# Optimization experiments

Measured on AMD Instinct MI355X. Metric: run time of the kernel, lower is better.

The kernel has to match this reference:

```python
import jax, jax.numpy as jnp
import numpy as np

B, A, N, G, F = 16, 256, 64, 64, 128  # batch, atoms, neighbors, gaussians, filters
CUTOFF = 5.0


def ssp(x):
    # shifted softplus: ln(0.5*e^x + 0.5)
    return jax.nn.softplus(x) - jnp.log(2.0).astype(x.dtype)


def setup_inputs() -> dict:
    key = jax.random.key(0)
    ks = jax.random.split(key, 10)
    x = jax.random.normal(ks[0], (B, A, F), jnp.float32)
    r_ij = jax.random.uniform(ks[1], (B, A, N), jnp.float32) * 6.0  # some beyond cutoff
    f_ij = jax.random.uniform(ks[2], (B, A, N, G), jnp.float32)  # gaussian-expanded dists
    neighbors = jax.random.randint(ks[3], (B, A, N), 0, A)
    pairwise_mask = (jax.random.uniform(ks[4], (B, A, N)) < 0.9).astype(jnp.float32)
    s = lambda fan: 1.0 / np.sqrt(fan)
    fw1 = jax.random.normal(ks[5], (G, F), jnp.float32) * s(G)
    fb1 = jnp.zeros((F,), jnp.float32)
    fw2 = jax.random.normal(ks[6], (F, F), jnp.float32) * s(F)
    fb2 = jnp.zeros((F,), jnp.float32)
    w_in2f = jax.random.normal(ks[7], (F, F), jnp.float32) * s(F)
    w_f2out = jax.random.normal(ks[8], (F, F), jnp.float32) * s(F)
    b_f2out = jnp.zeros((F,), jnp.float32)
    return {"x": x, "r_ij": r_ij, "f_ij": f_ij, "neighbors": neighbors,
            "pairwise_mask": pairwise_mask, "fw1": fw1, "fb1": fb1, "fw2": fw2,
            "fb2": fb2, "w_in2f": w_in2f, "w_f2out": w_f2out, "b_f2out": b_f2out}


def reference(x, r_ij, f_ij, neighbors, pairwise_mask,
              fw1, fb1, fw2, fb2, w_in2f, w_f2out, b_f2out):
    # filter network: Dense(G->F, ssp) -> Dense(F->F)
    W = ssp(jnp.einsum('bang,gf->banf', f_ij, fw1) + fb1)
    W = jnp.einsum('banf,fh->banh', W, fw2) + fb2  # [B,A,N,F]
    # cosine cutoff
    C = 0.5 * (jnp.cos(r_ij * (jnp.pi / CUTOFF)) + 1.0)
    C = C * (r_ij < CUTOFF).astype(r_ij.dtype)
    W = W * C[..., None]
    # in2f (no bias), then gather neighbor features along atom axis
    y = jnp.einsum('bad,df->baf', x, w_in2f)  # [B,A,F]
    bidx = jnp.arange(y.shape[0])[:, None, None]
    y_nbh = y[bidx, neighbors]  # [B,A,N,F]
    # filter-weight multiply + masked sum aggregate over neighbor axis
    y = jnp.sum(y_nbh * W * pairwise_mask[..., None], axis=2)  # [B,A,F]
    # f2out with shifted-softplus activation
    return ssp(jnp.einsum('baf,fo->bao', y, w_f2out) + b_f2out)
```

## Files before the change

kernel.cpp:

```cpp
#include <hip/hip_runtime.h>
#include <hip/hip_bf16.h>
#include <math.h>

#define B_ 16
#define A_ 256
#define N_ 64
#define G_ 64
#define F_ 128

typedef __attribute__((ext_vector_type(8))) short short8;
typedef __attribute__((ext_vector_type(4))) float floatx4;

__device__ __forceinline__ float ssp(float x) {
    const float t = __expf(-fabsf(x));
    return fmaxf(x, 0.0f) + __logf(1.0f + t) - 0.69314718055994531f;
}
__device__ __forceinline__ unsigned short f2bf(float f) {
    union { float f; unsigned u; } v; v.f = f;
    v.u += 0x7fffu + ((v.u >> 16) & 1u);
    return (unsigned short)(v.u >> 16);
}
__device__ __forceinline__ float bf2f(unsigned short u) {
    union { unsigned i; float f; } v;
    v.i = ((unsigned)u) << 16;
    return v.f;
}

__global__ __launch_bounds__(256) void k1_prep_in2f(
    const float* __restrict__ x,   const float* __restrict__ win,
    const float* __restrict__ fw1, const float* __restrict__ fw2,
    const float* __restrict__ wout,
    unsigned short* __restrict__ ypre,
    unsigned short* __restrict__ fw1B, unsigned short* __restrict__ fw2B,
    unsigned short* __restrict__ woutB)
{
    const int bid = blockIdx.x;
    const int tid = threadIdx.x;

    if (bid >= 256) {
        int idx = (bid - 256) * 1024 + tid * 4;
        #pragma unroll
        for (int u = 0; u < 4; ++u, ++idx) {
            if (idx < 8192) {
                const int j  = idx & 7;
                const int l  = (idx >> 3) & 63;
                const int ks = (idx >> 9) & 1;
                const int tf = idx >> 10;
                const int g  = ks * 32 + (l >> 4) * 8 + j;
                const int f  = tf * 16 + (l & 15);
                fw1B[idx] = f2bf(fw1[g * F_ + f]);
            } else {
                const int i2 = (idx - 8192) & 16383;
                const int sel = (idx - 8192) >> 14;
                const int j  = i2 & 7;
                const int l  = (i2 >> 3) & 63;
                const int ks = (i2 >> 9) & 3;
                const int tf = i2 >> 11;
                const int k  = ks * 32 + (l >> 4) * 8 + j;
                const int f  = tf * 16 + (l & 15);
                if (sel == 0) fw2B[i2]  = f2bf(fw2[k * F_ + f]);
                else          woutB[i2] = f2bf(wout[k * F_ + f]);
            }
        }
        return;
    }

    __shared__ unsigned short s_wt[128 * 136];

    const float4* win4 = (const float4*)win;
    for (int i = tid; i < 4096; i += 256) {
        const float4 v = win4[i];
        const int e = i * 4;
        const int k = e >> 7;
        const int f = e & 127;
        s_wt[(f + 0) * 136 + k] = f2bf(v.x);
        s_wt[(f + 1) * 136 + k] = f2bf(v.y);
        s_wt[(f + 2) * 136 + k] = f2bf(v.z);
        s_wt[(f + 3) * 136 + k] = f2bf(v.w);
    }
    __syncthreads();

    const int w = tid >> 6, l = tid & 63, quad = l >> 4, c0 = l & 15;
    const int row0 = bid * 16;

    short8 a[4];
    {
        const float* base = x + (size_t)(row0 + c0) * F_ + quad * 8;
        #pragma unroll
        for (int ks = 0; ks < 4; ++ks) {
            const float4 v0 = *(const float4*)(base + ks * 32);
            const float4 v1 = *(const float4*)(base + ks * 32 + 4);
            short8 t;
            t[0] = f2bf(v0.x); t[1] = f2bf(v0.y);
            t[2] = f2bf(v0.z); t[3] = f2bf(v0.w);
            t[4] = f2bf(v1.x); t[5] = f2bf(v1.y);
            t[6] = f2bf(v1.z); t[7] = f2bf(v1.w);
            a[ks] = t;
        }
    }

    floatx4 acc[2];
    acc[0] = (floatx4){0.f,0.f,0.f,0.f};
    acc[1] = (floatx4){0.f,0.f,0.f,0.f};
    #pragma unroll
    for (int t = 0; t < 2; ++t) {
        const int tf = w * 2 + t;
        #pragma unroll
        for (int ks = 0; ks < 4; ++ks) {
            const short8 bfrag = *(const short8*)
                &s_wt[(tf * 16 + c0) * 136 + ks * 32 + quad * 8];
            acc[t] = __builtin_amdgcn_mfma_f32_16x16x32_bf16(
                a[ks], bfrag, acc[t], 0, 0, 0);
        }
    }
    #pragma unroll
    for (int t = 0; t < 2; ++t) {
        const int tf = w * 2 + t;
        #pragma unroll
        for (int r = 0; r < 4; ++r)
            ypre[(size_t)(row0 + quad * 4 + r) * F_ + tf * 16 + c0] =
                f2bf(acc[t][r]);
    }
}

__global__ __launch_bounds__(256) void cfconv_kernel(
    const float* __restrict__ r_ij, const float* __restrict__ f_ij,
    const int*   __restrict__ nbrs, const float* __restrict__ mask,
    const float* __restrict__ fb1,  const float* __restrict__ fb2,
    const unsigned short* __restrict__ ypre,
    const unsigned short* __restrict__ fw1B,
    const unsigned short* __restrict__ fw2B,
    const unsigned short* __restrict__ woutB,
    const float* __restrict__ bf2out,
    float* __restrict__ out)
{
    __shared__ short s_h1[N_ * F_];
    __shared__ float s_scale[N_];
    __shared__ int   s_nb[N_];
    __shared__ float s_red[4][F_];
    __shared__ unsigned short s_yfb[F_];

    const int blk  = blockIdx.x;
    const int tid  = threadIdx.x;
    const int b    = blk >> 8;
    const int w    = tid >> 6;
    const int l    = tid & 63;
    const int quad = l >> 4;
    const int c0   = l & 15;

    if (l < 16) {
        const int n = w * 16 + l;
        const float r = r_ij[(size_t)blk * N_ + n];
        const float c = (r < 5.0f)
            ? 0.5f * (__cosf(r * 0.62831853071795865f) + 1.0f)
            : 0.0f;
        s_scale[n] = c * mask[(size_t)blk * N_ + n];
        s_nb[n]    = nbrs[(size_t)blk * N_ + n];
    }

    const short8* fw1B8  = (const short8*)fw1B;
    const short8* fw2B8  = (const short8*)fw2B;
    const short8* woutB8 = (const short8*)woutB;

    short8 a1[2];
    {
        const float* base = f_ij + (size_t)blk * (N_ * G_)
                          + (size_t)(w * 16 + c0) * G_ + quad * 8;
        #pragma unroll
        for (int ks = 0; ks < 2; ++ks) {
            const float4 v0 = *(const float4*)(base + ks * 32);
            const float4 v1 = *(const float4*)(base + ks * 32 + 4);
            short8 a;
            a[0] = f2bf(v0.x); a[1] = f2bf(v0.y);
            a[2] = f2bf(v0.z); a[3] = f2bf(v0.w);
            a[4] = f2bf(v1.x); a[5] = f2bf(v1.y);
            a[6] = f2bf(v1.z); a[7] = f2bf(v1.w);
            a1[ks] = a;
        }
    }
    floatx4 acc1[8];
    #pragma unroll
    for (int tf = 0; tf < 8; ++tf) acc1[tf] = (floatx4){0.f,0.f,0.f,0.f};
    #pragma unroll
    for (int ks = 0; ks < 2; ++ks)
        #pragma unroll
        for (int tf = 0; tf < 8; ++tf)
            acc1[tf] = __builtin_amdgcn_mfma_f32_16x16x32_bf16(
                a1[ks], fw1B8[(tf * 2 + ks) * 64 + l], acc1[tf], 0, 0, 0);

    #pragma unroll
    for (int tf = 0; tf < 8; ++tf) {
        const float bias  = fb1[tf * 16 + c0];
        const int   chunk = tf * 2 + (c0 >> 3);
        const int   o     = c0 & 7;
        #pragma unroll
        for (int r = 0; r < 4; ++r) {
            const int row_l = quad * 4 + r;
            const float v = ssp(acc1[tf][r] + bias);
            s_h1[(w * 16 + row_l) * F_ + ((chunk ^ row_l) * 8) + o] =
                (short)f2bf(v);
        }
    }

    short8 a2[4];
    #pragma unroll
    for (int ks = 0; ks < 4; ++ks)
        a2[ks] = *(const short8*)&s_h1[(w * 16 + c0) * F_
                                       + (((ks * 4 + quad) ^ c0) * 8)];

    int   rowoff[4];
    float scl[4];
    #pragma unroll
    for (int r = 0; r < 4; ++r) {
        const int n = w * 16 + quad * 4 + r;
        scl[r]    = s_scale[n];
        rowoff[r] = (b * A_ + s_nb[n]) * F_;
    }
    unsigned short yv[4][8];
    #pragma unroll
    for (int r = 0; r < 4; ++r)
        #pragma unroll
        for (int tf = 0; tf < 8; ++tf)
            yv[r][tf] = ypre[rowoff[r] + tf * 16 + c0];

    floatx4 acc2[8];
    #pragma unroll
    for (int tf = 0; tf < 8; ++tf) acc2[tf] = (floatx4){0.f,0.f,0.f,0.f};
    #pragma unroll
    for (int ks = 0; ks < 4; ++ks)
        #pragma unroll
        for (int tf = 0; tf < 8; ++tf)
            acc2[tf] = __builtin_amdgcn_mfma_f32_16x16x32_bf16(
                a2[ks], fw2B8[(tf * 4 + ks) * 64 + l], acc2[tf], 0, 0, 0);

    float part[8];
    #pragma unroll
    for (int tf = 0; tf < 8; ++tf) part[tf] = 0.0f;
    #pragma unroll
    for (int r = 0; r < 4; ++r)
        #pragma unroll
        for (int tf = 0; tf < 8; ++tf)
            part[tf] = fmaf((acc2[tf][r] + fb2[tf * 16 + c0]) * scl[r],
                            bf2f(yv[r][tf]), part[tf]);

    #pragma unroll
    for (int tf = 0; tf < 8; ++tf) {
        part[tf] += __shfl_xor(part[tf], 16, 64);
        part[tf] += __shfl_xor(part[tf], 32, 64);
    }
    if (l < 16) {
        #pragma unroll
        for (int tf = 0; tf < 8; ++tf)
            s_red[w][tf * 16 + l] = part[tf];
    }
    __syncthreads();

    if (tid < F_) {
        const float v = s_red[0][tid] + s_red[1][tid]
                      + s_red[2][tid] + s_red[3][tid];
        s_yfb[tid] = f2bf(v);
    }
    __syncthreads();

    short8 ya[4];
    #pragma unroll
    for (int ks = 0; ks < 4; ++ks)
        ya[ks] = *(const short8*)&s_yfb[ks * 32 + quad * 8];

    floatx4 aco[2];
    aco[0] = (floatx4){0.f,0.f,0.f,0.f};
    aco[1] = (floatx4){0.f,0.f,0.f,0.f};
    #pragma unroll
    for (int t = 0; t < 2; ++t) {
        const int tf = w * 2 + t;
        #pragma unroll
        for (int ks = 0; ks < 4; ++ks)
            aco[t] = __builtin_amdgcn_mfma_f32_16x16x32_bf16(
                ya[ks], woutB8[(tf * 4 + ks) * 64 + l], aco[t], 0, 0, 0);
    }
    if (quad == 0) {
        #pragma unroll
        for (int t = 0; t < 2; ++t) {
            const int c = (w * 2 + t) * 16 + c0;
            out[(size_t)blk * F_ + c] = ssp(aco[t][0] + bf2out[c]);
        }
    }
}

extern "C" void kernel_launch(void* const* d_in, const int* in_sizes, int n_in,
                              void* d_out, int out_size, void* d_ws, size_t ws_size,
                              hipStream_t stream) {
    const float* x        = (const float*)d_in[0];
    const float* r_ij     = (const float*)d_in[1];
    const float* f_ij     = (const float*)d_in[2];
    const int*   nbrs     = (const int*)  d_in[3];
    const float* mask     = (const float*)d_in[4];
    const float* fw1      = (const float*)d_in[5];
    const float* fb1      = (const float*)d_in[6];
    const float* fw2      = (const float*)d_in[7];
    const float* fb2      = (const float*)d_in[8];
    const float* w_in2f   = (const float*)d_in[9];
    const float* w_f2out  = (const float*)d_in[10];
    const float* b_f2out  = (const float*)d_in[11];
    float* out = (float*)d_out;

    unsigned short* ypre  = (unsigned short*)d_ws;
    unsigned short* fw1B  = ypre  + (size_t)B_ * A_ * F_;
    unsigned short* fw2B  = fw1B  + 8192;
    unsigned short* woutB = fw2B  + 16384;

    k1_prep_in2f<<<296, 256, 0, stream>>>(
        x, w_in2f, fw1, fw2, w_f2out, ypre, fw1B, fw2B, woutB);
    cfconv_kernel<<<B_ * A_, 256, 0, stream>>>(
        r_ij, f_ij, nbrs, mask, fb1, fb2,
        ypre, fw1B, fw2B, woutB, b_f2out, out);
}
```

Before: 166.8 us.

## Split f2out into batched GEMM kernel and vectorize gathered ypre loads

The final f2out projection moves out of the per-atom conv kernel into a separate kernel that runs full 16-row MFMA tiles over the aggregated features. Before, each block ran MFMAs on a single row and kept only one row of the result. ypre is also stored in an interleaved layout, so each lane gathers its 8 neighbour features with one 16-byte load instead of eight scalar 2-byte loads. The cost is an extra launch and a bf16 round trip of the aggregated features through global memory.

```diff
diff --git a/kernel.cpp b/kernel.cpp
--- a/kernel.cpp
+++ b/kernel.cpp
@@ -15,15 +15,16 @@
     const float t = __expf(-fabsf(x));
     return fmaxf(x, 0.0f) + __logf(1.0f + t) - 0.69314718055994531f;
 }
-__device__ __forceinline__ unsigned short f2bf(float f) {
+__device__ __forceinline__ unsigned f2bf(float f) {
     union { float f; unsigned u; } v; v.f = f;
     v.u += 0x7fffu + ((v.u >> 16) & 1u);
-    return (unsigned short)(v.u >> 16);
-}
-__device__ __forceinline__ float bf2f(unsigned short u) {
-    union { unsigned i; float f; } v;
-    v.i = ((unsigned)u) << 16;
-    return v.f;
+    return v.u >> 16;
+}
+__device__ __forceinline__ float bf2f_lo(unsigned d) {
+    union { unsigned i; float f; } v; v.i = d << 16; return v.f;
+}
+__device__ __forceinline__ float bf2f_hi(unsigned d) {
+    union { unsigned i; float f; } v; v.i = d & 0xffff0000u; return v.f;
 }
 
 __global__ __launch_bounds__(256) void k1_prep_in2f(
@@ -48,7 +49,7 @@
                 const int tf = idx >> 10;
                 const int g  = ks * 32 + (l >> 4) * 8 + j;
                 const int f  = tf * 16 + (l & 15);
-                fw1B[idx] = f2bf(fw1[g * F_ + f]);
+                fw1B[idx] = (unsigned short)f2bf(fw1[g * F_ + f]);
             } else {
                 const int i2 = (idx - 8192) & 16383;
                 const int sel = (idx - 8192) >> 14;
@@ -58,8 +59,8 @@
                 const int tf = i2 >> 11;
                 const int k  = ks * 32 + (l >> 4) * 8 + j;
                 const int f  = tf * 16 + (l & 15);
-                if (sel == 0) fw2B[i2]  = f2bf(fw2[k * F_ + f]);
-                else          woutB[i2] = f2bf(wout[k * F_ + f]);
+                if (sel == 0) fw2B[i2]  = (unsigned short)f2bf(fw2[k * F_ + f]);
+                else          woutB[i2] = (unsigned short)f2bf(wout[k * F_ + f]);
             }
         }
         return;
@@ -73,10 +74,10 @@
         const int e = i * 4;
         const int k = e >> 7;
         const int f = e & 127;
-        s_wt[(f + 0) * 136 + k] = f2bf(v.x);
-        s_wt[(f + 1) * 136 + k] = f2bf(v.y);
-        s_wt[(f + 2) * 136 + k] = f2bf(v.z);
-        s_wt[(f + 3) * 136 + k] = f2bf(v.w);
+        s_wt[(f + 0) * 136 + k] = (unsigned short)f2bf(v.x);
+        s_wt[(f + 1) * 136 + k] = (unsigned short)f2bf(v.y);
+        s_wt[(f + 2) * 136 + k] = (unsigned short)f2bf(v.z);
+        s_wt[(f + 3) * 136 + k] = (unsigned short)f2bf(v.w);
     }
     __syncthreads();
 
@@ -91,10 +92,10 @@
             const float4 v0 = *(const float4*)(base + ks * 32);
             const float4 v1 = *(const float4*)(base + ks * 32 + 4);
             short8 t;
-            t[0] = f2bf(v0.x); t[1] = f2bf(v0.y);
-            t[2] = f2bf(v0.z); t[3] = f2bf(v0.w);
-            t[4] = f2bf(v1.x); t[5] = f2bf(v1.y);
-            t[6] = f2bf(v1.z); t[7] = f2bf(v1.w);
+            t[0] = (short)f2bf(v0.x); t[1] = (short)f2bf(v0.y);
+            t[2] = (short)f2bf(v0.z); t[3] = (short)f2bf(v0.w);
+            t[4] = (short)f2bf(v1.x); t[5] = (short)f2bf(v1.y);
+            t[6] = (short)f2bf(v1.z); t[7] = (short)f2bf(v1.w);
             a[ks] = t;
         }
     }
@@ -114,12 +115,11 @@
         }
     }
     #pragma unroll
-    for (int t = 0; t < 2; ++t) {
-        const int tf = w * 2 + t;
-        #pragma unroll
-        for (int r = 0; r < 4; ++r)
-            ypre[(size_t)(row0 + quad * 4 + r) * F_ + tf * 16 + c0] =
-                f2bf(acc[t][r]);
+    for (int r = 0; r < 4; ++r) {
+        const int ro = row0 + quad * 4 + r;
+        const unsigned lo = f2bf(acc[0][r]);
+        const unsigned hi = f2bf(acc[1][r]);
+        *(unsigned*)&ypre[(size_t)ro * F_ + c0 * 8 + w * 2] = lo | (hi << 16);
     }
 }
 
@@ -130,15 +130,12 @@
     const unsigned short* __restrict__ ypre,
     const unsigned short* __restrict__ fw1B,
     const unsigned short* __restrict__ fw2B,
-    const unsigned short* __restrict__ woutB,
-    const float* __restrict__ bf2out,
-    float* __restrict__ out)
+    unsigned short* __restrict__ y_agg)
 {
     __shared__ short s_h1[N_ * F_];
     __shared__ float s_scale[N_];
     __shared__ int   s_nb[N_];
     __shared__ float s_red[4][F_];
-    __shared__ unsigned short s_yfb[F_];
 
     const int blk  = blockIdx.x;
     const int tid  = threadIdx.x;
@@ -158,9 +155,8 @@
         s_nb[n]    = nbrs[(size_t)blk * N_ + n];
     }
 
-    const short8* fw1B8  = (const short8*)fw1B;
-    const short8* fw2B8  = (const short8*)fw2B;
-    const short8* woutB8 = (const short8*)woutB;
+    const short8* fw1B8 = (const short8*)fw1B;
+    const short8* fw2B8 = (const short8*)fw2B;
 
     short8 a1[2];
     {
@@ -171,10 +167,10 @@
             const float4 v0 = *(const float4*)(base + ks * 32);
             const float4 v1 = *(const float4*)(base + ks * 32 + 4);
             short8 a;
-            a[0] = f2bf(v0.x); a[1] = f2bf(v0.y);
-            a[2] = f2bf(v0.z); a[3] = f2bf(v0.w);
-            a[4] = f2bf(v1.x); a[5] = f2bf(v1.y);
-            a[6] = f2bf(v1.z); a[7] = f2bf(v1.w);
+            a[0] = (short)f2bf(v0.x); a[1] = (short)f2bf(v0.y);
+            a[2] = (short)f2bf(v0.z); a[3] = (short)f2bf(v0.w);
+            a[4] = (short)f2bf(v1.x); a[5] = (short)f2bf(v1.y);
+            a[6] = (short)f2bf(v1.z); a[7] = (short)f2bf(v1.w);
             a1[ks] = a;
         }
     }
@@ -208,20 +204,14 @@
         a2[ks] = *(const short8*)&s_h1[(w * 16 + c0) * F_
                                        + (((ks * 4 + quad) ^ c0) * 8)];
 
-    int   rowoff[4];
     float scl[4];
+    uint4 yv[4];
     #pragma unroll
     for (int r = 0; r < 4; ++r) {
         const int n = w * 16 + quad * 4 + r;
-        scl[r]    = s_scale[n];
-        rowoff[r] = (b * A_ + s_nb[n]) * F_;
-    }
-    unsigned short yv[4][8];
-    #pragma unroll
-    for (int r = 0; r < 4; ++r)
-        #pragma unroll
-        for (int tf = 0; tf < 8; ++tf)
-            yv[r][tf] = ypre[rowoff[r] + tf * 16 + c0];
+        scl[r] = s_scale[n];
+        yv[r] = *(const uint4*)&ypre[(size_t)(b * A_ + s_nb[n]) * F_ + c0 * 8];
+    }
 
     floatx4 acc2[8];
     #pragma unroll
@@ -237,11 +227,17 @@
     #pragma unroll
     for (int tf = 0; tf < 8; ++tf) part[tf] = 0.0f;
     #pragma unroll
-    for (int r = 0; r < 4; ++r)
-        #pragma unroll
-        for (int tf = 0; tf < 8; ++tf)
-            part[tf] = fmaf((acc2[tf][r] + fb2[tf * 16 + c0]) * scl[r],
-                            bf2f(yv[r][tf]), part[tf]);
+    for (int r = 0; r < 4; ++r) {
+        const unsigned d0 = yv[r].x, d1 = yv[r].y, d2 = yv[r].z, d3 = yv[r].w;
+        part[0] = fmaf((acc2[0][r] + fb2[0*16+c0]) * scl[r], bf2f_lo(d0), part[0]);
+        part[1] = fmaf((acc2[1][r] + fb2[1*16+c0]) * scl[r], bf2f_hi(d0), part[1]);
+        part[2] = fmaf((acc2[2][r] + fb2[2*16+c0]) * scl[r], bf2f_lo(d1), part[2]);
+        part[3] = fmaf((acc2[3][r] + fb2[3*16+c0]) * scl[r], bf2f_hi(d1), part[3]);
+        part[4] = fmaf((acc2[4][r] + fb2[4*16+c0]) * scl[r], bf2f_lo(d2), part[4]);
+        part[5] = fmaf((acc2[5][r] + fb2[5*16+c0]) * scl[r], bf2f_hi(d2), part[5]);
+        part[6] = fmaf((acc2[6][r] + fb2[6*16+c0]) * scl[r], bf2f_lo(d3), part[6]);
+        part[7] = fmaf((acc2[7][r] + fb2[7*16+c0]) * scl[r], bf2f_hi(d3), part[7]);
+    }
 
     #pragma unroll
     for (int tf = 0; tf < 8; ++tf) {
@@ -258,31 +254,42 @@
     if (tid < F_) {
         const float v = s_red[0][tid] + s_red[1][tid]
                       + s_red[2][tid] + s_red[3][tid];
-        s_yfb[tid] = f2bf(v);
-    }
-    __syncthreads();
-
-    short8 ya[4];
+        y_agg[(size_t)blk * F_ + tid] = (unsigned short)f2bf(v);
+    }
+}
+
+__global__ __launch_bounds__(256) void f2out_kernel(
+    const unsigned short* __restrict__ y_agg,
+    const unsigned short* __restrict__ woutB,
+    const float* __restrict__ bias, float* __restrict__ out)
+{
+    const int tid = threadIdx.x;
+    const int w = tid >> 6, l = tid & 63, quad = l >> 4, c0 = l & 15;
+    const int row = blockIdx.x * 64 + w * 16 + c0;
+
+    short8 a[4];
     #pragma unroll
     for (int ks = 0; ks < 4; ++ks)
-        ya[ks] = *(const short8*)&s_yfb[ks * 32 + quad * 8];
-
-    floatx4 aco[2];
-    aco[0] = (floatx4){0.f,0.f,0.f,0.f};
-    aco[1] = (floatx4){0.f,0.f,0.f,0.f};
-    #pragma unroll
-    for (int t = 0; t < 2; ++t) {
-        const int tf = w * 2 + t;
-        #pragma unroll
-        for (int ks = 0; ks < 4; ++ks)
-            aco[t] = __builtin_amdgcn_mfma_f32_16x16x32_bf16(
-                ya[ks], woutB8[(tf * 4 + ks) * 64 + l], aco[t], 0, 0, 0);
-    }
-    if (quad == 0) {
-        #pragma unroll
-        for (int t = 0; t < 2; ++t) {
-            const int c = (w * 2 + t) * 16 + c0;
-            out[(size_t)blk * F_ + c] = ssp(aco[t][0] + bf2out[c]);
+        a[ks] = *(const short8*)&y_agg[(size_t)row * F_ + ks * 32 + quad * 8];
+
+    const short8* W8 = (const short8*)woutB;
+    floatx4 acc[8];
+    #pragma unroll
+    for (int tf = 0; tf < 8; ++tf) acc[tf] = (floatx4){0.f,0.f,0.f,0.f};
+    #pragma unroll
+    for (int ks = 0; ks < 4; ++ks)
+        #pragma unroll
+        for (int tf = 0; tf < 8; ++tf)
+            acc[tf] = __builtin_amdgcn_mfma_f32_16x16x32_bf16(
+                a[ks], W8[(tf * 4 + ks) * 64 + l], acc[tf], 0, 0, 0);
+
+    #pragma unroll
+    for (int tf = 0; tf < 8; ++tf) {
+        const float bs = bias[tf * 16 + c0];
+        #pragma unroll
+        for (int r = 0; r < 4; ++r) {
+            const int ro = blockIdx.x * 64 + w * 16 + quad * 4 + r;
+            out[(size_t)ro * F_ + tf * 16 + c0] = ssp(acc[tf][r] + bs);
         }
     }
 }
@@ -308,10 +315,11 @@
     unsigned short* fw1B  = ypre  + (size_t)B_ * A_ * F_;
     unsigned short* fw2B  = fw1B  + 8192;
     unsigned short* woutB = fw2B  + 16384;
+    unsigned short* y_agg = woutB + 16384;
 
     k1_prep_in2f<<<296, 256, 0, stream>>>(
         x, w_in2f, fw1, fw2, w_f2out, ypre, fw1B, fw2B, woutB);
     cfconv_kernel<<<B_ * A_, 256, 0, stream>>>(
-        r_ij, f_ij, nbrs, mask, fb1, fb2,
-        ypre, fw1B, fw2B, woutB, b_f2out, out);
-}
+        r_ij, f_ij, nbrs, mask, fb1, fb2, ypre, fw1B, fw2B, y_agg);
+    f2out_kernel<<<B_ * A_ / 64, 256, 0, stream>>>(y_agg, woutB, b_f2out, out);
+}
```

Measured after the change: 164.1 us. About the same (-1.6%).
